# Kernel optimization log

Hardware: AMD Instinct MI355X
Metric: run time of the kernel (lower is better)

The kernel has to match this reference:

```python
import jax, jax.numpy as jnp
import numpy as np

N_NODES, N_EDGES, F_IN, H1, H2, N_CLASSES = 10000, 640000, 128, 64, 32, 16


def gcn_conv(x, W, b, src, dst, n_nodes):
    """PyG GCNConv: x' = D^{-1/2} (A + I) D^{-1/2} (x W) + b, deg from dst + self-loop."""
    h = x @ W  # [N, out]
    deg = jax.ops.segment_sum(jnp.ones(src.shape[0], h.dtype), dst,
                              num_segments=n_nodes) + 1.0  # +1 self-loop
    dinv = jax.lax.rsqrt(deg)  # [N]
    coef = dinv[src] * dinv[dst]  # [E]
    agg = jax.ops.segment_sum(h[src] * coef[:, None], dst, num_segments=n_nodes)
    agg = agg + h * (dinv * dinv)[:, None]  # self-loop contribution
    return agg + b


def setup_inputs() -> dict:
    key = jax.random.key(0)
    ks = jax.random.split(key, 8)
    x = jax.random.normal(ks[0], (N_NODES, F_IN), jnp.float32)
    edge_index = jax.random.randint(ks[1], (2, N_EDGES), 0, N_NODES, jnp.int32)
    W1 = jax.random.normal(ks[2], (F_IN, H1), jnp.float32) / np.sqrt(F_IN)
    b1 = jnp.zeros((H1,), jnp.float32)
    W2 = jax.random.normal(ks[3], (H1, H2), jnp.float32) / np.sqrt(H1)
    b2 = jnp.zeros((H2,), jnp.float32)
    Wfc = jax.random.normal(ks[4], (H2, N_CLASSES), jnp.float32) / np.sqrt(H2)
    bfc = jnp.zeros((N_CLASSES,), jnp.float32)
    return {"x": x, "W1": W1, "b1": b1, "W2": W2, "b2": b2,
            "Wfc": Wfc, "bfc": bfc, "edge_index": edge_index}


def reference(x, W1, b1, W2, b2, Wfc, bfc, edge_index):
    src, dst = edge_index[0], edge_index[1]
    n = x.shape[0]
    h = jax.nn.relu(gcn_conv(x, W1, b1, src, dst, n))
    # dropout p=0.5 is identity in eval mode
    h = jax.nn.relu(gcn_conv(h, W2, b2, src, dst, n))
    g = jnp.mean(h, axis=0)  # [H2]
    return g @ Wfc + bfc  # [num_classes]
```

## Files before the change

kernel.cpp:

```cpp
#include <hip/hip_runtime.h>
#include <hip/hip_bf16.h>

#define N_NODES 10000
#define N_EDGES 640000
#define F_IN 128
#define H1 64
#define H2 32
#define N_CLASSES 16

#define NB 256
#define NPB 40
#define STAGE_C 32
#define PART_BLOCKS 313
#define CAP 3072
#define MAXDEG 128
#define GEMM_TILES 625

typedef unsigned short ushortT;
typedef unsigned long long u64T;

__device__ __forceinline__ float bf_lo(unsigned u) {
    u <<= 16; float f; __builtin_memcpy(&f, &u, 4); return f;
}
__device__ __forceinline__ float bf_hi(unsigned u) {
    u &= 0xffff0000u; float f; __builtin_memcpy(&f, &u, 4); return f;
}
__device__ __forceinline__ unsigned bf_pack(float a, float b) {
    __hip_bfloat16 ha = __float2bfloat16(a), hb = __float2bfloat16(b);
    unsigned short ua, ub;
    __builtin_memcpy(&ua, &ha, 2); __builtin_memcpy(&ub, &hb, 2);
    return (unsigned)ua | ((unsigned)ub << 16);
}

__global__ void __launch_bounds__(256) k_part_gemm1(const int* __restrict__ src,
                                                    const int* __restrict__ dst,
                                                    int* __restrict__ gcnt,
                                                    int* __restrict__ partBuf,
                                                    const float* __restrict__ x,
                                                    const float* __restrict__ W1,
                                                    __hip_bfloat16* __restrict__ h1b,
                                                    const float* __restrict__ bfc,
                                                    float* __restrict__ out) {
    __shared__ __align__(16) char pool[40960];
    int t = threadIdx.x;
    if (blockIdx.x < PART_BLOCKS) {
        int g = blockIdx.x;
        int* cnt   = (int*)pool;
        int* stage = (int*)(pool + 1024);
        if (t < NB) cnt[t] = 0;
        __syncthreads();
        const int4* src4 = (const int4*)src;
        const int4* dst4 = (const int4*)dst;
#pragma unroll
        for (int k = 0; k < 2; ++k) {
            int i4 = g * 512 + k * 256 + t;
            if (i4 < N_EDGES / 4) {
                int4 s = src4[i4];
                int4 d = dst4[i4];
                int b, l, p;
                b = d.x / NPB; l = d.x - b * NPB; p = atomicAdd(&cnt[b], 1);
                if (p < STAGE_C) stage[(b << 5) + p] = s.x | (l << 14);
                b = d.y / NPB; l = d.y - b * NPB; p = atomicAdd(&cnt[b], 1);
                if (p < STAGE_C) stage[(b << 5) + p] = s.y | (l << 14);
                b = d.z / NPB; l = d.z - b * NPB; p = atomicAdd(&cnt[b], 1);
                if (p < STAGE_C) stage[(b << 5) + p] = s.z | (l << 14);
                b = d.w / NPB; l = d.w - b * NPB; p = atomicAdd(&cnt[b], 1);
                if (p < STAGE_C) stage[(b << 5) + p] = s.w | (l << 14);
            }
        }
        __syncthreads();
        if (t < NB) {
            int c = cnt[t]; if (c > STAGE_C) c = STAGE_C;
            cnt[t] = c;
            gcnt[g * NB + t] = c;
        }
        __syncthreads();
#pragma unroll
        for (int rep = 0; rep < (NB * STAGE_C) / 256; ++rep) {
            int i = rep * 256 + t;
            int b = i >> 5, k = i & 31;
            if (k < cnt[b]) partBuf[(b * PART_BLOCKS + g) * STAGE_C + k] = stage[i];
        }
    } else {
        int gb = blockIdx.x - PART_BLOCKS;
        float4* w1q = (float4*)pool;
        float*  xs  = (float*)(pool + 32768);
        int node0 = gb * 16;
#pragma unroll
        for (int i = 0; i < 8; ++i) {
            int pair = i * 256 + t;
            int k4 = pair >> 6, j = pair & 63;
            int gb0 = k4 * 256 + j;
            w1q[pair] = make_float4(W1[gb0], W1[gb0 + 64], W1[gb0 + 128], W1[gb0 + 192]);
        }
        const float4* x4 = (const float4*)(x + (long)node0 * F_IN);
        float4* xs4w = (float4*)xs;
#pragma unroll
        for (int i = 0; i < 2; ++i) xs4w[i * 256 + t] = x4[i * 256 + t];
        if (gb == 0 && t < N_CLASSES) out[t] = bfc[t];
        __syncthreads();
        int j = t & 63;
        int q = t >> 6;
        int r0 = q * 4;
        const float4* xs4 = (const float4*)xs;
        float acc0 = 0.f, acc1 = 0.f, acc2 = 0.f, acc3 = 0.f;
#pragma unroll 8
        for (int k4 = 0; k4 < 32; ++k4) {
            float4 w = w1q[k4 * 64 + j];
            float4 a = xs4[(r0 + 0) * 32 + k4];
            float4 b = xs4[(r0 + 1) * 32 + k4];
            float4 c = xs4[(r0 + 2) * 32 + k4];
            float4 d = xs4[(r0 + 3) * 32 + k4];
            acc0 += a.x * w.x + a.y * w.y + a.z * w.z + a.w * w.w;
            acc1 += b.x * w.x + b.y * w.y + b.z * w.z + b.w * w.w;
            acc2 += c.x * w.x + c.y * w.y + c.z * w.z + c.w * w.w;
            acc3 += d.x * w.x + d.y * w.y + d.z * w.z + d.w * w.w;
        }
        int v0 = node0 + r0;
        h1b[(v0 + 0) * H1 + j] = __float2bfloat16(acc0);
        h1b[(v0 + 1) * H1 + j] = __float2bfloat16(acc1);
        h1b[(v0 + 2) * H1 + j] = __float2bfloat16(acc2);
        h1b[(v0 + 3) * H1 + j] = __float2bfloat16(acc3);
    }
}

__global__ void __launch_bounds__(512) k_place(const int* __restrict__ gcnt,
                                               const int* __restrict__ partBuf,
                                               int* __restrict__ cnt,
                                               ushortT* __restrict__ adj,
                                               float* __restrict__ dinv,
                                               __hip_bfloat16* __restrict__ h1b) {
    __shared__ int scnt[PART_BLOCKS];
    __shared__ int pre[PART_BLOCKS + 1];
    __shared__ int dense[CAP];
    __shared__ int ldeg[NPB];
    __shared__ int cur[NPB];
    __shared__ float sdv[NPB];
    int t = threadIdx.x;
    int b = blockIdx.x;
    int nodeBase = b * NPB;
    if (t < PART_BLOCKS) scnt[t] = gcnt[t * NB + b];
    if (t < NPB) ldeg[t] = 0;
    __syncthreads();
    if (t < PART_BLOCKS) pre[t + 1] = scnt[t];
    if (t == 0) pre[0] = 0;
    __syncthreads();
    for (int off = 1; off < PART_BLOCKS; off <<= 1) {
        int v = 0;
        if (t >= off && t < PART_BLOCKS) v = pre[t + 1 - off];
        __syncthreads();
        if (t >= off && t < PART_BLOCKS) pre[t + 1] += v;
        __syncthreads();
    }
    int tot = pre[PART_BLOCKS]; if (tot > CAP) tot = CAP;
    if (t < PART_BLOCKS) {
        int c = scnt[t], base = pre[t];
        const int* rp = partBuf + (b * PART_BLOCKS + t) * STAGE_C;
        for (int k = 0; k < c; ++k) {
            int dd = base + k;
            if (dd < CAP) dense[dd] = rp[k];
        }
    }
    __syncthreads();
    for (int i = t; i < tot; i += 512)
        atomicAdd(&ldeg[dense[i] >> 14], 1);
    __syncthreads();
    if (t < NPB) {
        int v = nodeBase + t;
        int c = ldeg[t];
        cnt[v] = c;
        float dv_ = rsqrtf((float)c + 1.0f);
        dinv[v] = dv_;
        sdv[t] = dv_;
        cur[t] = 0;
    }
    __syncthreads();
    for (int i = t; i < tot; i += 512) {
        int p = dense[i];
        int ln = p >> 14;
        int pos = atomicAdd(&cur[ln], 1);
        if (pos < MAXDEG) adj[(nodeBase + ln) * MAXDEG + pos] = (ushortT)(p & 16383);
    }
    unsigned* h1u = (unsigned*)h1b;
    for (int i = t; i < NPB * 32; i += 512) {
        int ln = i >> 5, pp = i & 31;
        int v = nodeBase + ln;
        unsigned u = h1u[v * 32 + pp];
        float d = sdv[ln];
        h1u[v * 32 + pp] = bf_pack(bf_lo(u) * d, bf_hi(u) * d);
    }
}

__global__ void __launch_bounds__(256) k_gather1_gemm2(const __hip_bfloat16* __restrict__ h1b,
                                const int* __restrict__ cnt,
                                const ushortT* __restrict__ adj,
                                const float* __restrict__ dinv,
                                const float* __restrict__ b1,
                                const float* __restrict__ W2,
                                __hip_bfloat16* __restrict__ h2b) {
    __shared__ float h1s[16 * 68];
    __shared__ __align__(16) ushortT idxs[16 * MAXDEG];
    __shared__ float w2s[H1 * H2];
    int t = threadIdx.x;
    int n = t >> 4;
    int l = t & 15;
    int v0 = blockIdx.x * 16;
    int v = v0 + n;
    const float4* W24 = (const float4*)W2;
    float4* w2s4 = (float4*)w2s;
#pragma unroll
    for (int i = 0; i < 2; ++i) w2s4[i * 256 + t] = W24[i * 256 + t];
    const unsigned* a32 = (const unsigned*)(adj + (long)v0 * MAXDEG);
    unsigned* i32 = (unsigned*)idxs;
#pragma unroll
    for (int i = 0; i < 4; ++i) i32[i * 256 + t] = a32[i * 256 + t];
    int deg = cnt[v]; if (deg > MAXDEG) deg = MAXDEG;
    float dv_ = dinv[v];
    const u64T* h164 = (const u64T*)h1b;
    u64T su = h164[v * 16 + l];
    unsigned slo = (unsigned)su, shi = (unsigned)(su >> 32);
    float f0 = bf_lo(slo), f1 = bf_hi(slo), f2 = bf_lo(shi), f3 = bf_hi(shi);
    float p0 = 0.f, p1 = 0.f, p2 = 0.f, p3 = 0.f;
    float q0 = 0.f, q1 = 0.f, q2 = 0.f, q3 = 0.f;
    __syncthreads();
    const ushortT* myRow = &idxs[n * MAXDEG];
    int e = 0;
    for (; e + 8 <= deg; e += 8) {
        int4 iv = *(const int4*)(myRow + e);
        int i0 = iv.x & 0xffff, i1 = (int)((unsigned)iv.x >> 16);
        int i2 = iv.y & 0xffff, i3 = (int)((unsigned)iv.y >> 16);
        int i4 = iv.z & 0xffff, i5 = (int)((unsigned)iv.z >> 16);
        int i6 = iv.w & 0xffff, i7 = (int)((unsigned)iv.w >> 16);
        u64T u0 = h164[i0 * 16 + l];
        u64T u1 = h164[i1 * 16 + l];
        u64T u2 = h164[i2 * 16 + l];
        u64T u3 = h164[i3 * 16 + l];
        u64T u4 = h164[i4 * 16 + l];
        u64T u5 = h164[i5 * 16 + l];
        u64T u6 = h164[i6 * 16 + l];
        u64T u7 = h164[i7 * 16 + l];
        unsigned lo, hi;
        lo = (unsigned)u0; hi = (unsigned)(u0 >> 32);
        p0 += bf_lo(lo); p1 += bf_hi(lo); p2 += bf_lo(hi); p3 += bf_hi(hi);
        lo = (unsigned)u1; hi = (unsigned)(u1 >> 32);
        q0 += bf_lo(lo); q1 += bf_hi(lo); q2 += bf_lo(hi); q3 += bf_hi(hi);
        lo = (unsigned)u2; hi = (unsigned)(u2 >> 32);
        p0 += bf_lo(lo); p1 += bf_hi(lo); p2 += bf_lo(hi); p3 += bf_hi(hi);
        lo = (unsigned)u3; hi = (unsigned)(u3 >> 32);
        q0 += bf_lo(lo); q1 += bf_hi(lo); q2 += bf_lo(hi); q3 += bf_hi(hi);
        lo = (unsigned)u4; hi = (unsigned)(u4 >> 32);
        p0 += bf_lo(lo); p1 += bf_hi(lo); p2 += bf_lo(hi); p3 += bf_hi(hi);
        lo = (unsigned)u5; hi = (unsigned)(u5 >> 32);
        q0 += bf_lo(lo); q1 += bf_hi(lo); q2 += bf_lo(hi); q3 += bf_hi(hi);
        lo = (unsigned)u6; hi = (unsigned)(u6 >> 32);
        p0 += bf_lo(lo); p1 += bf_hi(lo); p2 += bf_lo(hi); p3 += bf_hi(hi);
        lo = (unsigned)u7; hi = (unsigned)(u7 >> 32);
        q0 += bf_lo(lo); q1 += bf_hi(lo); q2 += bf_lo(hi); q3 += bf_hi(hi);
    }
    for (; e < deg; ++e) {
        u64T u = h164[myRow[e] * 16 + l];
        unsigned lo = (unsigned)u, hi = (unsigned)(u >> 32);
        p0 += bf_lo(lo); p1 += bf_hi(lo); p2 += bf_lo(hi); p3 += bf_hi(hi);
    }
    f0 += p0 + q0; f1 += p1 + q1; f2 += p2 + q2; f3 += p3 + q3;
    float4 bb = ((const float4*)b1)[l];
    float4 r;
    r.x = fmaxf(dv_ * f0 + bb.x, 0.f);
    r.y = fmaxf(dv_ * f1 + bb.y, 0.f);
    r.z = fmaxf(dv_ * f2 + bb.z, 0.f);
    r.w = fmaxf(dv_ * f3 + bb.w, 0.f);
    ((float4*)(h1s + n * 68))[l] = r;
    __syncthreads();
    float acc0 = 0.f, acc1 = 0.f;
#pragma unroll
    for (int kk = 0; kk < H1; ++kk) {
        float hv = h1s[n * 68 + kk];
        float2 w = ((const float2*)(w2s + kk * H2))[l];
        acc0 += hv * w.x;
        acc1 += hv * w.y;
    }
    ((unsigned*)h2b)[v * 16 + l] = bf_pack(acc0 * dv_, acc1 * dv_);
}

__global__ void __launch_bounds__(256) k_gather2_out(const __hip_bfloat16* __restrict__ h2b,
                               const int* __restrict__ cnt,
                               const ushortT* __restrict__ adj,
                               const float* __restrict__ dinv,
                               const float* __restrict__ b2,
                               const float* __restrict__ Wfc,
                               float* __restrict__ out) {
    __shared__ float red[32 * 36];
    __shared__ __align__(16) ushortT idxs[32 * MAXDEG];
    __shared__ float gs[H2];
    int t = threadIdx.x;
    int n = t >> 3;
    int l = t & 7;
    int v0 = blockIdx.x * 32;
    int v = v0 + n;
    bool valid = v < N_NODES;
    const unsigned* a32 = (const unsigned*)(adj + (long)v0 * MAXDEG);
    unsigned* i32 = (unsigned*)idxs;
#pragma unroll
    for (int i = 0; i < 8; ++i) i32[i * 256 + t] = a32[i * 256 + t];
    int deg = valid ? cnt[v] : 0; if (deg > MAXDEG) deg = MAXDEG; if (deg < 0) deg = 0;
    float dv_ = valid ? dinv[v] : 0.f;
    const u64T* h264 = (const u64T*)h2b;
    u64T su = valid ? h264[v * 8 + l] : 0ull;
    unsigned slo = (unsigned)su, shi = (unsigned)(su >> 32);
    float f0 = bf_lo(slo), f1 = bf_hi(slo), f2 = bf_lo(shi), f3 = bf_hi(shi);
    float p0 = 0.f, p1 = 0.f, p2 = 0.f, p3 = 0.f;
    float q0 = 0.f, q1 = 0.f, q2 = 0.f, q3 = 0.f;
    __syncthreads();
    const ushortT* myRow = &idxs[n * MAXDEG];
    int e = 0;
    for (; e + 8 <= deg; e += 8) {
        int4 iv = *(const int4*)(myRow + e);
        int i0 = iv.x & 0xffff, i1 = (int)((unsigned)iv.x >> 16);
        int i2 = iv.y & 0xffff, i3 = (int)((unsigned)iv.y >> 16);
        int i4 = iv.z & 0xffff, i5 = (int)((unsigned)iv.z >> 16);
        int i6 = iv.w & 0xffff, i7 = (int)((unsigned)iv.w >> 16);
        u64T u0 = h264[i0 * 8 + l];
        u64T u1 = h264[i1 * 8 + l];
        u64T u2 = h264[i2 * 8 + l];
        u64T u3 = h264[i3 * 8 + l];
        u64T u4 = h264[i4 * 8 + l];
        u64T u5 = h264[i5 * 8 + l];
        u64T u6 = h264[i6 * 8 + l];
        u64T u7 = h264[i7 * 8 + l];
        unsigned lo, hi;
        lo = (unsigned)u0; hi = (unsigned)(u0 >> 32);
        p0 += bf_lo(lo); p1 += bf_hi(lo); p2 += bf_lo(hi); p3 += bf_hi(hi);
        lo = (unsigned)u1; hi = (unsigned)(u1 >> 32);
        q0 += bf_lo(lo); q1 += bf_hi(lo); q2 += bf_lo(hi); q3 += bf_hi(hi);
        lo = (unsigned)u2; hi = (unsigned)(u2 >> 32);
        p0 += bf_lo(lo); p1 += bf_hi(lo); p2 += bf_lo(hi); p3 += bf_hi(hi);
        lo = (unsigned)u3; hi = (unsigned)(u3 >> 32);
        q0 += bf_lo(lo); q1 += bf_hi(lo); q2 += bf_lo(hi); q3 += bf_hi(hi);
        lo = (unsigned)u4; hi = (unsigned)(u4 >> 32);
        p0 += bf_lo(lo); p1 += bf_hi(lo); p2 += bf_lo(hi); p3 += bf_hi(hi);
        lo = (unsigned)u5; hi = (unsigned)(u5 >> 32);
        q0 += bf_lo(lo); q1 += bf_hi(lo); q2 += bf_lo(hi); q3 += bf_hi(hi);
        lo = (unsigned)u6; hi = (unsigned)(u6 >> 32);
        p0 += bf_lo(lo); p1 += bf_hi(lo); p2 += bf_lo(hi); p3 += bf_hi(hi);
        lo = (unsigned)u7; hi = (unsigned)(u7 >> 32);
        q0 += bf_lo(lo); q1 += bf_hi(lo); q2 += bf_lo(hi); q3 += bf_hi(hi);
    }
    for (; e < deg; ++e) {
        u64T u = h264[myRow[e] * 8 + l];
        unsigned lo = (unsigned)u, hi = (unsigned)(u >> 32);
        p0 += bf_lo(lo); p1 += bf_hi(lo); p2 += bf_lo(hi); p3 += bf_hi(hi);
    }
    f0 += p0 + q0; f1 += p1 + q1; f2 += p2 + q2; f3 += p3 + q3;
    float4 bb = ((const float4*)b2)[l];
    float4 r;
    r.x = fmaxf(dv_ * f0 + bb.x, 0.f);
    r.y = fmaxf(dv_ * f1 + bb.y, 0.f);
    r.z = fmaxf(dv_ * f2 + bb.z, 0.f);
    r.w = fmaxf(dv_ * f3 + bb.w, 0.f);
    if (!valid) { r.x = 0.f; r.y = 0.f; r.z = 0.f; r.w = 0.f; }
    ((float4*)(red + n * 36))[l] = r;
    __syncthreads();
    if (t < H2) {
        float s = 0.f;
#pragma unroll
        for (int rr = 0; rr < 32; ++rr) s += red[rr * 36 + t];
        gs[t] = s;
    }
    __syncthreads();
    if (t < N_CLASSES) {
        float acc = 0.f;
#pragma unroll
        for (int j = 0; j < H2; ++j)
            acc += gs[j] * Wfc[j * N_CLASSES + t];
        atomicAdd(&out[t], acc * (1.0f / (float)N_NODES));
    }
}

extern "C" void kernel_launch(void* const* d_in, const int* in_sizes, int n_in,
                              void* d_out, int out_size, void* d_ws, size_t ws_size,
                              hipStream_t stream) {
    const float* x   = (const float*)d_in[0];
    const float* W1  = (const float*)d_in[1];
    const float* b1  = (const float*)d_in[2];
    const float* W2  = (const float*)d_in[3];
    const float* b2  = (const float*)d_in[4];
    const float* Wfc = (const float*)d_in[5];
    const float* bfc = (const float*)d_in[6];
    const int* edge  = (const int*)d_in[7];
    const int* srcI = edge;
    const int* dstI = edge + N_EDGES;
    float* out = (float*)d_out;

    char* ws = (char*)d_ws;
    int*     gcnt    = (int*)    (ws + 0);
    int*     cnt     = (int*)    (ws + 321536);
    float*   dinv    = (float*)  (ws + 362496);
    int*     partBuf = (int*)    (ws + 403456);
    ushortT* adj     = (ushortT*)(ws + 10659840);
    __hip_bfloat16* h1b = (__hip_bfloat16*)(ws + 13223936);
    __hip_bfloat16* h2b = (__hip_bfloat16*)(ws + 14503936);

    k_part_gemm1<<<PART_BLOCKS + GEMM_TILES, 256, 0, stream>>>(
        srcI, dstI, gcnt, partBuf, x, W1, h1b, bfc, out);
    k_place<<<250, 512, 0, stream>>>(gcnt, partBuf, cnt, adj, dinv, h1b);
    k_gather1_gemm2<<<625, 256, 0, stream>>>(h1b, cnt, adj, dinv, b1, W2, h2b);
    k_gather2_out<<<313, 256, 0, stream>>>(h2b, cnt, adj, dinv, b2, Wfc, out);
}
```

Before: 112.8 us.

## Split each node's neighbor gather across multiple thread groups with shared-memory reduction

Both gather kernels now assign 2 (layer 1) or 4 (layer 2) thread groups per destination node. Each group handles an interleaved subset of the 8-edge chunks, and the partial sums are combined through a shared-memory buffer. Block sizes grow to 512 and 1024 threads. The layer-2 GEMM is remapped so each of 512 threads computes one output feature. The goal is more memory-level parallelism and shorter per-thread dependency chains on the latency-bound gathers, at the cost of extra synchronisation, shared memory, and possibly lower occupancy with larger blocks.

```diff
diff --git a/kernel.cpp b/kernel.cpp
--- a/kernel.cpp
+++ b/kernel.cpp
@@ -191,7 +191,7 @@
     }
 }
 
-__global__ void __launch_bounds__(256) k_gather1_gemm2(const __hip_bfloat16* __restrict__ h1b,
+__global__ void __launch_bounds__(512) k_gather1_gemm2(const __hip_bfloat16* __restrict__ h1b,
                                 const int* __restrict__ cnt,
                                 const ushortT* __restrict__ adj,
                                 const float* __restrict__ dinv,
@@ -201,32 +201,34 @@
     __shared__ float h1s[16 * 68];
     __shared__ __align__(16) ushortT idxs[16 * MAXDEG];
     __shared__ float w2s[H1 * H2];
+    __shared__ float4 pbuf[16 * 2 * 16];
     int t = threadIdx.x;
-    int n = t >> 4;
+    int n = t >> 5;
+    int half = (t >> 4) & 1;
     int l = t & 15;
     int v0 = blockIdx.x * 16;
     int v = v0 + n;
-    const float4* W24 = (const float4*)W2;
-    float4* w2s4 = (float4*)w2s;
-#pragma unroll
-    for (int i = 0; i < 2; ++i) w2s4[i * 256 + t] = W24[i * 256 + t];
+    ((float4*)w2s)[t] = ((const float4*)W2)[t];
     const unsigned* a32 = (const unsigned*)(adj + (long)v0 * MAXDEG);
     unsigned* i32 = (unsigned*)idxs;
-#pragma unroll
-    for (int i = 0; i < 4; ++i) i32[i * 256 + t] = a32[i * 256 + t];
+    i32[t] = a32[t];
+    i32[512 + t] = a32[512 + t];
     int deg = cnt[v]; if (deg > MAXDEG) deg = MAXDEG;
     float dv_ = dinv[v];
     const u64T* h164 = (const u64T*)h1b;
-    u64T su = h164[v * 16 + l];
-    unsigned slo = (unsigned)su, shi = (unsigned)(su >> 32);
-    float f0 = bf_lo(slo), f1 = bf_hi(slo), f2 = bf_lo(shi), f3 = bf_hi(shi);
+    float f0 = 0.f, f1 = 0.f, f2 = 0.f, f3 = 0.f;
+    if (half == 0) {
+        u64T su = h164[v * 16 + l];
+        unsigned slo = (unsigned)su, shi = (unsigned)(su >> 32);
+        f0 = bf_lo(slo); f1 = bf_hi(slo); f2 = bf_lo(shi); f3 = bf_hi(shi);
+    }
     float p0 = 0.f, p1 = 0.f, p2 = 0.f, p3 = 0.f;
     float q0 = 0.f, q1 = 0.f, q2 = 0.f, q3 = 0.f;
     __syncthreads();
     const ushortT* myRow = &idxs[n * MAXDEG];
-    int e = 0;
-    for (; e + 8 <= deg; e += 8) {
-        int4 iv = *(const int4*)(myRow + e);
+    int F = deg >> 3;
+    for (int r = half; r < F; r += 2) {
+        int4 iv = *(const int4*)(myRow + r * 8);
         int i0 = iv.x & 0xffff, i1 = (int)((unsigned)iv.x >> 16);
         int i2 = iv.y & 0xffff, i3 = (int)((unsigned)iv.y >> 16);
         int i4 = iv.z & 0xffff, i5 = (int)((unsigned)iv.z >> 16);
@@ -257,32 +259,38 @@
         lo = (unsigned)u7; hi = (unsigned)(u7 >> 32);
         q0 += bf_lo(lo); q1 += bf_hi(lo); q2 += bf_lo(hi); q3 += bf_hi(hi);
     }
-    for (; e < deg; ++e) {
-        u64T u = h164[myRow[e] * 16 + l];
-        unsigned lo = (unsigned)u, hi = (unsigned)(u >> 32);
-        p0 += bf_lo(lo); p1 += bf_hi(lo); p2 += bf_lo(hi); p3 += bf_hi(hi);
+    if (half == (F & 1)) {
+        for (int e = F * 8; e < deg; ++e) {
+            u64T u = h164[myRow[e] * 16 + l];
+            unsigned lo = (unsigned)u, hi = (unsigned)(u >> 32);
+            p0 += bf_lo(lo); p1 += bf_hi(lo); p2 += bf_lo(hi); p3 += bf_hi(hi);
+        }
     }
     f0 += p0 + q0; f1 += p1 + q1; f2 += p2 + q2; f3 += p3 + q3;
-    float4 bb = ((const float4*)b1)[l];
-    float4 r;
-    r.x = fmaxf(dv_ * f0 + bb.x, 0.f);
-    r.y = fmaxf(dv_ * f1 + bb.y, 0.f);
-    r.z = fmaxf(dv_ * f2 + bb.z, 0.f);
-    r.w = fmaxf(dv_ * f3 + bb.w, 0.f);
-    ((float4*)(h1s + n * 68))[l] = r;
-    __syncthreads();
-    float acc0 = 0.f, acc1 = 0.f;
-#pragma unroll
-    for (int kk = 0; kk < H1; ++kk) {
-        float hv = h1s[n * 68 + kk];
-        float2 w = ((const float2*)(w2s + kk * H2))[l];
-        acc0 += hv * w.x;
-        acc1 += hv * w.y;
-    }
-    ((unsigned*)h2b)[v * 16 + l] = bf_pack(acc0 * dv_, acc1 * dv_);
-}
-
-__global__ void __launch_bounds__(256) k_gather2_out(const __hip_bfloat16* __restrict__ h2b,
+    pbuf[(n * 2 + half) * 16 + l] = make_float4(f0, f1, f2, f3);
+    __syncthreads();
+    if (half == 0) {
+        float4 a = pbuf[(n * 2 + 0) * 16 + l];
+        float4 b = pbuf[(n * 2 + 1) * 16 + l];
+        float4 bb = ((const float4*)b1)[l];
+        float4 r;
+        r.x = fmaxf(dv_ * (a.x + b.x) + bb.x, 0.f);
+        r.y = fmaxf(dv_ * (a.y + b.y) + bb.y, 0.f);
+        r.z = fmaxf(dv_ * (a.z + b.z) + bb.z, 0.f);
+        r.w = fmaxf(dv_ * (a.w + b.w) + bb.w, 0.f);
+        ((float4*)(h1s + n * 68))[l] = r;
+    }
+    __syncthreads();
+    int j = t & 31;
+    int n2 = t >> 5;
+    float acc = 0.f;
+#pragma unroll
+    for (int kk = 0; kk < H1; ++kk)
+        acc += h1s[n2 * 68 + kk] * w2s[kk * H2 + j];
+    h2b[(v0 + n2) * H2 + j] = __float2bfloat16(acc * dinv[v0 + n2]);
+}
+
+__global__ void __launch_bounds__(1024) k_gather2_out(const __hip_bfloat16* __restrict__ h2b,
                                const int* __restrict__ cnt,
                                const ushortT* __restrict__ adj,
                                const float* __restrict__ dinv,
@@ -291,30 +299,35 @@
                                float* __restrict__ out) {
     __shared__ float red[32 * 36];
     __shared__ __align__(16) ushortT idxs[32 * MAXDEG];
+    __shared__ float4 pbuf[32 * 4 * 8];
     __shared__ float gs[H2];
     int t = threadIdx.x;
-    int n = t >> 3;
+    int n = t >> 5;
+    int quar = (t >> 3) & 3;
     int l = t & 7;
     int v0 = blockIdx.x * 32;
     int v = v0 + n;
     bool valid = v < N_NODES;
     const unsigned* a32 = (const unsigned*)(adj + (long)v0 * MAXDEG);
     unsigned* i32 = (unsigned*)idxs;
-#pragma unroll
-    for (int i = 0; i < 8; ++i) i32[i * 256 + t] = a32[i * 256 + t];
+    i32[t] = a32[t];
+    i32[1024 + t] = a32[1024 + t];
     int deg = valid ? cnt[v] : 0; if (deg > MAXDEG) deg = MAXDEG; if (deg < 0) deg = 0;
     float dv_ = valid ? dinv[v] : 0.f;
     const u64T* h264 = (const u64T*)h2b;
-    u64T su = valid ? h264[v * 8 + l] : 0ull;
-    unsigned slo = (unsigned)su, shi = (unsigned)(su >> 32);
-    float f0 = bf_lo(slo), f1 = bf_hi(slo), f2 = bf_lo(shi), f3 = bf_hi(shi);
+    float f0 = 0.f, f1 = 0.f, f2 = 0.f, f3 = 0.f;
+    if (quar == 0 && valid) {
+        u64T su = h264[v * 8 + l];
+        unsigned slo = (unsigned)su, shi = (unsigned)(su >> 32);
+        f0 = bf_lo(slo); f1 = bf_hi(slo); f2 = bf_lo(shi); f3 = bf_hi(shi);
+    }
     float p0 = 0.f, p1 = 0.f, p2 = 0.f, p3 = 0.f;
     float q0 = 0.f, q1 = 0.f, q2 = 0.f, q3 = 0.f;
     __syncthreads();
     const ushortT* myRow = &idxs[n * MAXDEG];
-    int e = 0;
-    for (; e + 8 <= deg; e += 8) {
-        int4 iv = *(const int4*)(myRow + e);
+    int F = deg >> 3;
+    for (int r = quar; r < F; r += 4) {
+        int4 iv = *(const int4*)(myRow + r * 8);
         int i0 = iv.x & 0xffff, i1 = (int)((unsigned)iv.x >> 16);
         int i2 = iv.y & 0xffff, i3 = (int)((unsigned)iv.y >> 16);
         int i4 = iv.z & 0xffff, i5 = (int)((unsigned)iv.z >> 16);
@@ -345,20 +358,30 @@
         lo = (unsigned)u7; hi = (unsigned)(u7 >> 32);
         q0 += bf_lo(lo); q1 += bf_hi(lo); q2 += bf_lo(hi); q3 += bf_hi(hi);
     }
-    for (; e < deg; ++e) {
-        u64T u = h264[myRow[e] * 8 + l];
-        unsigned lo = (unsigned)u, hi = (unsigned)(u >> 32);
-        p0 += bf_lo(lo); p1 += bf_hi(lo); p2 += bf_lo(hi); p3 += bf_hi(hi);
+    if (quar == (F & 3)) {
+        for (int e = F * 8; e < deg; ++e) {
+            u64T u = h264[myRow[e] * 8 + l];
+            unsigned lo = (unsigned)u, hi = (unsigned)(u >> 32);
+            p0 += bf_lo(lo); p1 += bf_hi(lo); p2 += bf_lo(hi); p3 += bf_hi(hi);
+        }
     }
     f0 += p0 + q0; f1 += p1 + q1; f2 += p2 + q2; f3 += p3 + q3;
-    float4 bb = ((const float4*)b2)[l];
-    float4 r;
-    r.x = fmaxf(dv_ * f0 + bb.x, 0.f);
-    r.y = fmaxf(dv_ * f1 + bb.y, 0.f);
-    r.z = fmaxf(dv_ * f2 + bb.z, 0.f);
-    r.w = fmaxf(dv_ * f3 + bb.w, 0.f);
-    if (!valid) { r.x = 0.f; r.y = 0.f; r.z = 0.f; r.w = 0.f; }
-    ((float4*)(red + n * 36))[l] = r;
+    pbuf[(n * 4 + quar) * 8 + l] = make_float4(f0, f1, f2, f3);
+    __syncthreads();
+    if (quar == 0) {
+        float4 a = pbuf[(n * 4 + 0) * 8 + l];
+        float4 b = pbuf[(n * 4 + 1) * 8 + l];
+        float4 c = pbuf[(n * 4 + 2) * 8 + l];
+        float4 d = pbuf[(n * 4 + 3) * 8 + l];
+        float4 bb = ((const float4*)b2)[l];
+        float4 r;
+        r.x = fmaxf(dv_ * (a.x + b.x + c.x + d.x) + bb.x, 0.f);
+        r.y = fmaxf(dv_ * (a.y + b.y + c.y + d.y) + bb.y, 0.f);
+        r.z = fmaxf(dv_ * (a.z + b.z + c.z + d.z) + bb.z, 0.f);
+        r.w = fmaxf(dv_ * (a.w + b.w + c.w + d.w) + bb.w, 0.f);
+        if (!valid) { r.x = 0.f; r.y = 0.f; r.z = 0.f; r.w = 0.f; }
+        ((float4*)(red + n * 36))[l] = r;
+    }
     __syncthreads();
     if (t < H2) {
         float s = 0.f;
@@ -403,6 +426,6 @@
     k_part_gemm1<<<PART_BLOCKS + GEMM_TILES, 256, 0, stream>>>(
         srcI, dstI, gcnt, partBuf, x, W1, h1b, bfc, out);
     k_place<<<250, 512, 0, stream>>>(gcnt, partBuf, cnt, adj, dinv, h1b);
-    k_gather1_gemm2<<<625, 256, 0, stream>>>(h1b, cnt, adj, dinv, b1, W2, h2b);
-    k_gather2_out<<<313, 256, 0, stream>>>(h2b, cnt, adj, dinv, b2, Wfc, out);
-}
+    k_gather1_gemm2<<<625, 512, 0, stream>>>(h1b, cnt, adj, dinv, b1, W2, h2b);
+    k_gather2_out<<<313, 1024, 0, stream>>>(h2b, cnt, adj, dinv, b2, Wfc, out);
+}
```

Measured after the change: 112.6 us. No clear change (-0.2%).
